# Kernel optimization log

Hardware: AMD Instinct MI355X
Metric: run time of the kernel (lower is better)

Reference implementation:

```python
import jax, jax.numpy as jnp
import numpy as np

EMBED_DIM = 1024
NUM_HEADS = 16
HEAD_DIM = EMBED_DIM // NUM_HEADS


def setup_inputs() -> dict:
    key = jax.random.key(0)
    ks = jax.random.split(key, 9)
    B, T, C = 2, 2048, EMBED_DIM
    s = 1.0 / np.sqrt(C)
    inp = {
        "x": jax.random.normal(ks[0], (B, T, C), dtype=jnp.float32),
        "Wq": jax.random.uniform(ks[1], (C, C), jnp.float32, -s, s),
        "bq": jax.random.uniform(ks[2], (C,), jnp.float32, -s, s),
        "Wk": jax.random.uniform(ks[3], (C, C), jnp.float32, -s, s),
        "bk": jax.random.uniform(ks[4], (C,), jnp.float32, -s, s),
        "Wv": jax.random.uniform(ks[5], (C, C), jnp.float32, -s, s),
        "bv": jax.random.uniform(ks[6], (C,), jnp.float32, -s, s),
        "Wo": jax.random.uniform(ks[7], (C, C), jnp.float32, -s, s),
        "bo": jax.random.uniform(ks[8], (C,), jnp.float32, -s, s),
    }
    return inp


def reference(x, Wq, bq, Wk, bk, Wv, bv, Wo, bo):
    B, T, C = x.shape
    H, D = NUM_HEADS, HEAD_DIM

    def heads(W, b):
        # [B,T,C] -> [B,H,T,D]
        return (x @ W + b).reshape(B, T, H, D).transpose(0, 2, 1, 3)

    q = heads(Wq, bq)
    k = heads(Wk, bk)
    v = heads(Wv, bv)

    scores = jnp.einsum('bhtd,bhsd->bhts', q, k) / np.sqrt(D).astype(np.float32)
    causal = jnp.tril(jnp.ones((T, T), dtype=bool))  # [T,T]
    scores = jnp.where(causal[None, None], scores, -jnp.inf)
    weights = jax.nn.softmax(scores, axis=-1)
    out = jnp.einsum('bhts,bhsd->bhtd', weights, v)  # [B,H,T,D]
    out = out.transpose(0, 2, 1, 3).reshape(B, T, C)
    return out @ Wo + bo
```

## Files before the change

kernel.cpp:

```cpp
#include <hip/hip_runtime.h>
#include <stdint.h>

#define T_LEN 2048
#define C_DIM 1024
#define NHEAD 16
#define HDIM  64
#define MTOT  4096

typedef __bf16 bf16;
typedef __bf16 bf16x4 __attribute__((ext_vector_type(4)));
typedef __bf16 bf16x8 __attribute__((ext_vector_type(8)));
typedef float  f32x4  __attribute__((ext_vector_type(4)));

__device__ __forceinline__ bf16 f2bf(float f) {
    union { float f; unsigned u; } x; x.f = f;
    unsigned r = x.u + 0x7fffu + ((x.u >> 16) & 1u);
    unsigned short h = (unsigned short)(r >> 16);
    return __builtin_bit_cast(bf16, h);
}

__device__ __forceinline__ void g2l16(const void* g, const void* l) {
    __builtin_amdgcn_global_load_lds(
        (const __attribute__((address_space(1))) unsigned int*)(uintptr_t)g,
        (__attribute__((address_space(3))) unsigned int*)(uint32_t)(uintptr_t)l,
        16, 0, 0);
}

__global__ void cast_xw_kernel(const float* __restrict__ x, bf16* __restrict__ xb,
                               const float* __restrict__ W0, const float* __restrict__ W1,
                               const float* __restrict__ W2, const float* __restrict__ W3,
                               bf16* __restrict__ wt) {
    __shared__ float tile[64][68];
    const int tid = threadIdx.x;
    const int bid = blockIdx.x;
    if (bid < 2048) {
        int f = bid * 256 + tid;
        const float4* p = (const float4*)x + (size_t)f * 2;
        float4 a = p[0], b = p[1];
        bf16x8 o;
        o[0] = f2bf(a.x); o[1] = f2bf(a.y); o[2] = f2bf(a.z); o[3] = f2bf(a.w);
        o[4] = f2bf(b.x); o[5] = f2bf(b.y); o[6] = f2bf(b.z); o[7] = f2bf(b.w);
        ((bf16x8*)xb)[f] = o;
        return;
    }
    const int i = bid - 2048;
    const int w = i >> 8;
    const int nt = (i >> 4) & 15;
    const int kt = i & 15;
    const float* W = (w == 0) ? W0 : (w == 1) ? W1 : (w == 2) ? W2 : W3;
    const int kb = kt * 64, nb = nt * 64;
#pragma unroll
    for (int pass = 0; pass < 4; ++pass) {
        int row = pass * 16 + (tid >> 4);
        int col = (tid & 15) * 4;
        float4 v = *(const float4*)(W + (size_t)(kb + row) * 1024 + nb + col);
        *(float4*)(&tile[row][col]) = v;
    }
    __syncthreads();
#pragma unroll
    for (int pass = 0; pass < 2; ++pass) {
        int s = pass * 256 + tid;
        int nn = s >> 3, c = s & 7;
        bf16x8 o;
#pragma unroll
        for (int j = 0; j < 8; ++j) o[j] = f2bf(tile[c * 8 + j][nn]);
        *(bf16x8*)(wt + (size_t)w * 1048576 + (size_t)(nb + nn) * 1024 + kb + c * 8) = o;
    }
}

__global__ void transpose_v_kernel(const bf16* __restrict__ V, bf16* __restrict__ Vtp) {
    __shared__ bf16 tile[128][72];
    const int tid = threadIdx.x;
    const int t0 = blockIdx.x * 128, bh = blockIdx.y;
    const size_t hb = (size_t)bh * 131072;
#pragma unroll
    for (int pass = 0; pass < 4; ++pass) {
        int s = pass * 256 + tid;
        int row = s >> 3, c = s & 7;
        bf16x8 v = *(const bf16x8*)(V + hb + (size_t)(t0 + row) * 64 + c * 8);
        *(bf16x8*)(&tile[row][c * 8]) = v;
    }
    __syncthreads();
#pragma unroll
    for (int pass = 0; pass < 4; ++pass) {
        int s = pass * 256 + tid;
        int d = s >> 4, ch = s & 15;
        bf16x8 o;
#pragma unroll
        for (int j = 0; j < 8; ++j) {
            int orig = 32 * (ch >> 2) + 16 * (j >> 2) + 4 * (ch & 3) + (j & 3);
            o[j] = tile[orig][d];
        }
        *(bf16x8*)(Vtp + hb + (size_t)d * 2048 + t0 + ch * 8) = o;
    }
}

__global__ __launch_bounds__(256, 2)
void gemm_qkv_kernel(const bf16* __restrict__ A, const bf16* __restrict__ Wt,
                     const float* __restrict__ b0, const float* __restrict__ b1,
                     const float* __restrict__ b2, bf16* __restrict__ outQKV) {
    __shared__ char lds[40960];
    bf16* As = (bf16*)lds;
    bf16* Bs = (bf16*)(lds + 16384);

    const int tid = threadIdx.x;
    const int lane = tid & 63, wid = tid >> 6;
    const int r = lane & 15, q4 = lane >> 4;
    const int mbase = blockIdx.y * 128;
    const int nbase = blockIdx.x * 192;
    const int wm = (wid >> 1) * 64;
    const int wn = (wid & 1) * 96;

    f32x4 acc[4][6];
#pragma unroll
    for (int i = 0; i < 4; ++i)
#pragma unroll
        for (int j = 0; j < 6; ++j) acc[i][j] = f32x4{0.f, 0.f, 0.f, 0.f};

    for (int kt = 0; kt < 16; ++kt) {
        int kb = kt * 64;
#pragma unroll
        for (int p = 0; p < 4; ++p) {
            int s = p * 256 + tid;
            int row = s >> 3, blk = s & 7;
            g2l16(A + (size_t)(mbase + row) * 1024 + kb + ((blk ^ (row & 7)) * 8), (char*)As + s * 16);
        }
#pragma unroll
        for (int p = 0; p < 6; ++p) {
            int s = p * 256 + tid;
            int row = s >> 3, blk = s & 7;
            g2l16(Wt + (size_t)(nbase + row) * 1024 + kb + ((blk ^ (row & 7)) * 8), (char*)Bs + s * 16);
        }
        __syncthreads();
#pragma unroll
        for (int ks = 0; ks < 2; ++ks) {
            int blk = ks * 4 + q4;
            bf16x8 a[4], b[6];
#pragma unroll
            for (int i = 0; i < 4; ++i) {
                int rowa = wm + i * 16 + r;
                a[i] = *(const bf16x8*)((const char*)As + rowa * 128 + ((blk ^ (rowa & 7)) * 16));
            }
#pragma unroll
            for (int j = 0; j < 6; ++j) {
                int rowb = wn + j * 16 + r;
                b[j] = *(const bf16x8*)((const char*)Bs + rowb * 128 + ((blk ^ (rowb & 7)) * 16));
            }
#pragma unroll
            for (int i = 0; i < 4; ++i)
#pragma unroll
                for (int j = 0; j < 6; ++j)
                    acc[i][j] = __builtin_amdgcn_mfma_f32_16x16x32_bf16(b[j], a[i], acc[i][j], 0, 0, 0);
        }
        __syncthreads();
    }

    const float QS = 0.18033688011112042f;
#pragma unroll
    for (int i = 0; i < 4; ++i) {
        int m = mbase + wm + i * 16 + r;
        int bi = m >> 11, t = m & 2047;
#pragma unroll
        for (int j = 0; j < 6; ++j) {
            int n0 = nbase + wn + j * 16 + q4 * 4;
            int z = n0 >> 10;
            int nz = n0 & 1023;
            const float* bias = (z == 0) ? b0 : (z == 1) ? b1 : b2;
            float4 bb = *(const float4*)(bias + nz);
            float osc = (z == 0) ? QS : 1.0f;
            bf16x4 w;
            w[0] = f2bf((acc[i][j][0] + bb.x) * osc);
            w[1] = f2bf((acc[i][j][1] + bb.y) * osc);
            w[2] = f2bf((acc[i][j][2] + bb.z) * osc);
            w[3] = f2bf((acc[i][j][3] + bb.w) * osc);
            int h = nz >> 6, d = nz & 63;
            *(bf16x4*)(outQKV + (size_t)z * 4194304 + ((size_t)(bi * 16 + h) * 2048 + t) * 64 + d) = w;
        }
    }
}

__global__ __launch_bounds__(128, 4)
void gemm_o_kernel(const bf16* __restrict__ A, const bf16* __restrict__ Bt,
                   const float* __restrict__ bias, float* __restrict__ out) {
    __shared__ char lds[16384];
    bf16* As = (bf16*)lds;
    bf16* Bs = (bf16*)(lds + 8192);

    const int tid = threadIdx.x;
    const int lane = tid & 63, wid = tid >> 6;
    const int r = lane & 15, q4 = lane >> 4;
    const int nb = blockIdx.x * 64;
    const int mb = blockIdx.y * 64;
    const int wn = wid * 32;

    float4 bvv[2];
#pragma unroll
    for (int j = 0; j < 2; ++j) bvv[j] = *(const float4*)(bias + nb + wn + j * 16 + q4 * 4);

    f32x4 acc[4][2];
#pragma unroll
    for (int i = 0; i < 4; ++i)
#pragma unroll
        for (int j = 0; j < 2; ++j) acc[i][j] = f32x4{0.f, 0.f, 0.f, 0.f};

    for (int kt = 0; kt < 16; ++kt) {
        int kb = kt * 64;
#pragma unroll
        for (int p = 0; p < 4; ++p) {
            int s = p * 128 + tid;
            int row = s >> 3, blk = s & 7;
            g2l16(A + (size_t)(mb + row) * 1024 + kb + ((blk ^ (row & 7)) * 8), (char*)As + s * 16);
        }
#pragma unroll
        for (int p = 0; p < 4; ++p) {
            int s = p * 128 + tid;
            int row = s >> 3, blk = s & 7;
            g2l16(Bt + (size_t)(nb + row) * 1024 + kb + ((blk ^ (row & 7)) * 8), (char*)Bs + s * 16);
        }
        __syncthreads();
#pragma unroll
        for (int ks = 0; ks < 2; ++ks) {
            int blk = ks * 4 + q4;
            bf16x8 a[4], b[2];
#pragma unroll
            for (int i = 0; i < 4; ++i) {
                int rowa = i * 16 + r;
                a[i] = *(const bf16x8*)((const char*)As + rowa * 128 + ((blk ^ (rowa & 7)) * 16));
            }
#pragma unroll
            for (int j = 0; j < 2; ++j) {
                int rowb = wn + j * 16 + r;
                b[j] = *(const bf16x8*)((const char*)Bs + rowb * 128 + ((blk ^ (rowb & 7)) * 16));
            }
#pragma unroll
            for (int i = 0; i < 4; ++i)
#pragma unroll
                for (int j = 0; j < 2; ++j)
                    acc[i][j] = __builtin_amdgcn_mfma_f32_16x16x32_bf16(b[j], a[i], acc[i][j], 0, 0, 0);
        }
        __syncthreads();
    }

#pragma unroll
    for (int i = 0; i < 4; ++i) {
        int m = mb + i * 16 + r;
#pragma unroll
        for (int j = 0; j < 2; ++j) {
            int n0 = nb + wn + j * 16 + q4 * 4;
            float4 w;
            w.x = acc[i][j][0] + bvv[j].x;
            w.y = acc[i][j][1] + bvv[j].y;
            w.z = acc[i][j][2] + bvv[j].z;
            w.w = acc[i][j][3] + bvv[j].w;
            *(float4*)(out + (size_t)m * 1024 + n0) = w;
        }
    }
}

__global__ __launch_bounds__(512, 2)
void attn_kernel(const bf16* __restrict__ Q, const bf16* __restrict__ K,
                 const bf16* __restrict__ Vtp, bf16* __restrict__ Aout) {
    __shared__ char lds[65536];

    const int tid = threadIdx.x, lane = tid & 63, wid = tid >> 6;
    const int r = lane & 15, q4 = lane >> 4;
    const int p = blockIdx.x >> 5;
    const int bh = blockIdx.x & 31;
    const int b = bh >> 4, h = bh & 15;
    const size_t hb = (size_t)bh * 131072;

    const int qi[2] = { p, 15 - p };
    const int ittot = 16 - p;

    bf16x8 qf[2][2];
#pragma unroll
    for (int i = 0; i < 2; ++i)
#pragma unroll
        for (int ks = 0; ks < 2; ++ks) {
            int row = qi[i] * 128 + wid * 16 + r;
            qf[i][ks] = *(const bf16x8*)(Q + hb + (size_t)row * 64 + ks * 32 + q4 * 8);
        }

    bf16x8 ones;
#pragma unroll
    for (int j = 0; j < 8; ++j) ones[j] = (bf16)1.0f;

    f32x4 o[2][4];
    f32x4 osum[2];
#pragma unroll
    for (int i = 0; i < 2; ++i) {
        osum[i] = f32x4{0.f, 0.f, 0.f, 0.f};
#pragma unroll
        for (int jd = 0; jd < 4; ++jd) o[i][jd] = f32x4{0.f, 0.f, 0.f, 0.f};
    }

    auto stage = [&](int buf, int kb) {
        char* Kb = lds + buf * 16384;
        char* Vb = lds + 32768 + buf * 16384;
#pragma unroll
        for (int pp = 0; pp < 2; ++pp) {
            int s = pp * 512 + tid;
            int row = s >> 3, blk = s & 7;
            g2l16(K + hb + (size_t)(kb + row) * 64 + ((blk ^ (row & 7)) * 8), Kb + s * 16);
        }
#pragma unroll
        for (int pp = 0; pp < 2; ++pp) {
            int s = pp * 512 + tid;
            int row = s >> 4, ch = s & 15;
            g2l16(Vtp + hb + (size_t)row * 2048 + kb + ((ch ^ (row & 15)) * 8), Vb + s * 16);
        }
    };

    stage(0, 0);

    for (int it = 0; it < ittot; ++it) {
        __syncthreads();
        const int cb = it & 1;
        if (it + 1 < ittot) stage((it + 1) & 1, (it + 1) * 128);
        const int kb = it * 128;
        const char* Kb = lds + cb * 16384;
        const char* Vb = lds + 32768 + cb * 16384;
        const bool aAct = (it <= qi[0]);

        f32x4 sc[2][8];
#pragma unroll
        for (int st = 0; st < 8; ++st) {
            int rowk = st * 16 + r;
            bf16x8 ak0 = *(const bf16x8*)(Kb + rowk * 128 + ((q4 ^ (rowk & 7)) * 16));
            bf16x8 ak1 = *(const bf16x8*)(Kb + rowk * 128 + (((4 + q4) ^ (rowk & 7)) * 16));
            sc[1][st] = __builtin_amdgcn_mfma_f32_16x16x32_bf16(ak0, qf[1][0], f32x4{0.f, 0.f, 0.f, 0.f}, 0, 0, 0);
            sc[1][st] = __builtin_amdgcn_mfma_f32_16x16x32_bf16(ak1, qf[1][1], sc[1][st], 0, 0, 0);
            if (aAct) {
                sc[0][st] = __builtin_amdgcn_mfma_f32_16x16x32_bf16(ak0, qf[0][0], f32x4{0.f, 0.f, 0.f, 0.f}, 0, 0, 0);
                sc[0][st] = __builtin_amdgcn_mfma_f32_16x16x32_bf16(ak1, qf[0][1], sc[0][st], 0, 0, 0);
            }
        }

#pragma unroll
        for (int i = 0; i < 2; ++i) {
            if (i == 0 && !aAct) continue;
            const bool dia = (it == qi[i]);
            int qrow = qi[i] * 128 + wid * 16 + r;
            bf16x8 pb[4];
#pragma unroll
            for (int c = 0; c < 4; ++c) {
                bf16x8 t;
                if (dia) {
#pragma unroll
                    for (int j = 0; j < 8; ++j) {
                        int st = 2 * c + (j >> 2), reg = j & 3;
                        int key = kb + st * 16 + q4 * 4 + reg;
                        float sv = (key > qrow) ? -1e30f : sc[i][st][reg];
                        t[j] = (bf16)__builtin_amdgcn_exp2f(sv);
                    }
                } else {
#pragma unroll
                    for (int j = 0; j < 8; ++j) {
                        int st = 2 * c + (j >> 2), reg = j & 3;
                        t[j] = (bf16)__builtin_amdgcn_exp2f(sc[i][st][reg]);
                    }
                }
                pb[c] = t;
            }
#pragma unroll
            for (int c = 0; c < 4; ++c) {
                int sidx = c * 4 + q4;
                osum[i] = __builtin_amdgcn_mfma_f32_16x16x32_bf16(ones, pb[c], osum[i], 0, 0, 0);
#pragma unroll
                for (int dsub = 0; dsub < 4; ++dsub) {
                    int rowd = dsub * 16 + r;
                    bf16x8 av = *(const bf16x8*)(Vb + rowd * 256 + ((sidx ^ (rowd & 15)) * 16));
                    o[i][dsub] = __builtin_amdgcn_mfma_f32_16x16x32_bf16(av, pb[c], o[i][dsub], 0, 0, 0);
                }
            }
        }
    }

#pragma unroll
    for (int i = 0; i < 2; ++i) {
        float inv = 1.f / osum[i][0];
        int q = qi[i] * 128 + wid * 16 + r;
#pragma unroll
        for (int dsub = 0; dsub < 4; ++dsub) {
            bf16x4 w;
#pragma unroll
            for (int reg = 0; reg < 4; ++reg) w[reg] = f2bf(o[i][dsub][reg] * inv);
            *(bf16x4*)(Aout + ((size_t)(b * 2048 + q)) * 1024 + h * 64 + dsub * 16 + q4 * 4) = w;
        }
    }
}


extern "C" void kernel_launch(void* const* d_in, const int* in_sizes, int n_in,
                              void* d_out, int out_size, void* d_ws, size_t ws_size,
                              hipStream_t stream) {
    const float* x  = (const float*)d_in[0];
    const float* Wq = (const float*)d_in[1];
    const float* bq = (const float*)d_in[2];
    const float* Wk = (const float*)d_in[3];
    const float* bk = (const float*)d_in[4];
    const float* Wv = (const float*)d_in[5];
    const float* bv = (const float*)d_in[6];
    const float* Wo = (const float*)d_in[7];
    const float* bo = (const float*)d_in[8];
    float* out = (float*)d_out;

    char* ws = (char*)d_ws;
    bf16* xb   = (bf16*)(ws);
    bf16* wt   = (bf16*)(ws + 8388608);
    bf16* qkv  = (bf16*)(ws + 16777216);
    bf16* vtp  = (bf16*)(ws + 41943040);
    bf16* attn = (bf16*)(ws + 50331648);

    hipLaunchKernelGGL(cast_xw_kernel, dim3(3072), dim3(256), 0, stream,
                       x, xb, Wq, Wk, Wv, Wo, wt);
    hipLaunchKernelGGL(gemm_qkv_kernel, dim3(16, 32), dim3(256), 0, stream,
                       xb, wt, bq, bk, bv, qkv);
    hipLaunchKernelGGL(transpose_v_kernel, dim3(16, 32), dim3(256), 0, stream,
                       qkv + (size_t)2 * 4194304, vtp);
    hipLaunchKernelGGL(attn_kernel, dim3(256), dim3(512), 0, stream,
                       qkv, qkv + 4194304, vtp, attn);
    hipLaunchKernelGGL(gemm_o_kernel, dim3(16, 64), dim3(128), 0, stream,
                       attn, wt + (size_t)3 * 1048576, bo, out);
}
```

Measured before the change: 170.7 us.

## Fuse V transpose into QKV GEMM epilogue and shrink attention tiles to 64

The QKV GEMM epilogue now writes V directly in the transposed, permuted layout the attention kernel reads, which removes the separate transpose kernel launch and its round trip through memory. The attention kernel moves from 128-row query/key tiles with 512 threads to 64-row tiles with 256 threads, launching twice as many blocks with half the LDS each. The V epilogue now issues scalar 2-byte strided stores instead of vector stores, and the smaller tiles double the number of loop iterations and barriers.

After: 170.2 us. About the same (-0.3%).

```diff
diff --git a/kernel.cpp b/kernel.cpp
--- a/kernel.cpp
+++ b/kernel.cpp
@@ -68,37 +68,11 @@
     }
 }
 
-__global__ void transpose_v_kernel(const bf16* __restrict__ V, bf16* __restrict__ Vtp) {
-    __shared__ bf16 tile[128][72];
-    const int tid = threadIdx.x;
-    const int t0 = blockIdx.x * 128, bh = blockIdx.y;
-    const size_t hb = (size_t)bh * 131072;
-#pragma unroll
-    for (int pass = 0; pass < 4; ++pass) {
-        int s = pass * 256 + tid;
-        int row = s >> 3, c = s & 7;
-        bf16x8 v = *(const bf16x8*)(V + hb + (size_t)(t0 + row) * 64 + c * 8);
-        *(bf16x8*)(&tile[row][c * 8]) = v;
-    }
-    __syncthreads();
-#pragma unroll
-    for (int pass = 0; pass < 4; ++pass) {
-        int s = pass * 256 + tid;
-        int d = s >> 4, ch = s & 15;
-        bf16x8 o;
-#pragma unroll
-        for (int j = 0; j < 8; ++j) {
-            int orig = 32 * (ch >> 2) + 16 * (j >> 2) + 4 * (ch & 3) + (j & 3);
-            o[j] = tile[orig][d];
-        }
-        *(bf16x8*)(Vtp + hb + (size_t)d * 2048 + t0 + ch * 8) = o;
-    }
-}
-
 __global__ __launch_bounds__(256, 2)
 void gemm_qkv_kernel(const bf16* __restrict__ A, const bf16* __restrict__ Wt,
                      const float* __restrict__ b0, const float* __restrict__ b1,
-                     const float* __restrict__ b2, bf16* __restrict__ outQKV) {
+                     const float* __restrict__ b2, bf16* __restrict__ outQKV,
+                     bf16* __restrict__ Vtp) {
     __shared__ char lds[40960];
     bf16* As = (bf16*)lds;
     bf16* Bs = (bf16*)(lds + 16384);
@@ -167,14 +141,24 @@
             int nz = n0 & 1023;
             const float* bias = (z == 0) ? b0 : (z == 1) ? b1 : b2;
             float4 bb = *(const float4*)(bias + nz);
-            float osc = (z == 0) ? QS : 1.0f;
-            bf16x4 w;
-            w[0] = f2bf((acc[i][j][0] + bb.x) * osc);
-            w[1] = f2bf((acc[i][j][1] + bb.y) * osc);
-            w[2] = f2bf((acc[i][j][2] + bb.z) * osc);
-            w[3] = f2bf((acc[i][j][3] + bb.w) * osc);
             int h = nz >> 6, d = nz & 63;
-            *(bf16x4*)(outQKV + (size_t)z * 4194304 + ((size_t)(bi * 16 + h) * 2048 + t) * 64 + d) = w;
+            if (z == 2) {
+                int tl = t & 127;
+                int tp = (tl & 96) | (((tl >> 2) & 3) << 3) | (((tl >> 4) & 1) << 2) | (tl & 3);
+                size_t base = (size_t)(bi * 16 + h) * 131072 + (size_t)(t & ~127) + tp;
+                Vtp[base + (size_t)(d + 0) * 2048] = f2bf(acc[i][j][0] + bb.x);
+                Vtp[base + (size_t)(d + 1) * 2048] = f2bf(acc[i][j][1] + bb.y);
+                Vtp[base + (size_t)(d + 2) * 2048] = f2bf(acc[i][j][2] + bb.z);
+                Vtp[base + (size_t)(d + 3) * 2048] = f2bf(acc[i][j][3] + bb.w);
+            } else {
+                float osc = (z == 0) ? QS : 1.0f;
+                bf16x4 w;
+                w[0] = f2bf((acc[i][j][0] + bb.x) * osc);
+                w[1] = f2bf((acc[i][j][1] + bb.y) * osc);
+                w[2] = f2bf((acc[i][j][2] + bb.z) * osc);
+                w[3] = f2bf((acc[i][j][3] + bb.w) * osc);
+                *(bf16x4*)(outQKV + (size_t)z * 4194304 + ((size_t)(bi * 16 + h) * 2048 + t) * 64 + d) = w;
+            }
         }
     }
 }
@@ -257,10 +241,10 @@
     }
 }
 
-__global__ __launch_bounds__(512, 2)
+__global__ __launch_bounds__(256, 2)
 void attn_kernel(const bf16* __restrict__ Q, const bf16* __restrict__ K,
                  const bf16* __restrict__ Vtp, bf16* __restrict__ Aout) {
-    __shared__ char lds[65536];
+    __shared__ char lds[32768];
 
     const int tid = threadIdx.x, lane = tid & 63, wid = tid >> 6;
     const int r = lane & 15, q4 = lane >> 4;
@@ -269,15 +253,15 @@
     const int b = bh >> 4, h = bh & 15;
     const size_t hb = (size_t)bh * 131072;
 
-    const int qi[2] = { p, 15 - p };
-    const int ittot = 16 - p;
+    const int qi[2] = { p, 31 - p };
+    const int ittot = 32 - p;
 
     bf16x8 qf[2][2];
 #pragma unroll
     for (int i = 0; i < 2; ++i)
 #pragma unroll
         for (int ks = 0; ks < 2; ++ks) {
-            int row = qi[i] * 128 + wid * 16 + r;
+            int row = qi[i] * 64 + wid * 16 + r;
             qf[i][ks] = *(const bf16x8*)(Q + hb + (size_t)row * 64 + ks * 32 + q4 * 8);
         }
 
@@ -296,18 +280,18 @@
 
     auto stage = [&](int buf, int kb) {
         char* Kb = lds + buf * 16384;
-        char* Vb = lds + 32768 + buf * 16384;
+        char* Vb = Kb + 8192;
 #pragma unroll
         for (int pp = 0; pp < 2; ++pp) {
-            int s = pp * 512 + tid;
+            int s = pp * 256 + tid;
             int row = s >> 3, blk = s & 7;
             g2l16(K + hb + (size_t)(kb + row) * 64 + ((blk ^ (row & 7)) * 8), Kb + s * 16);
         }
 #pragma unroll
         for (int pp = 0; pp < 2; ++pp) {
-            int s = pp * 512 + tid;
-            int row = s >> 4, ch = s & 15;
-            g2l16(Vtp + hb + (size_t)row * 2048 + kb + ((ch ^ (row & 15)) * 8), Vb + s * 16);
+            int s = pp * 256 + tid;
+            int row = s >> 3, ch = s & 7;
+            g2l16(Vtp + hb + (size_t)row * 2048 + kb + ((ch ^ (row & 7)) * 8), Vb + s * 16);
         }
     };
 
@@ -316,15 +300,15 @@
     for (int it = 0; it < ittot; ++it) {
         __syncthreads();
         const int cb = it & 1;
-        if (it + 1 < ittot) stage((it + 1) & 1, (it + 1) * 128);
-        const int kb = it * 128;
+        if (it + 1 < ittot) stage(cb ^ 1, (it + 1) * 64);
+        const int kb = it * 64;
         const char* Kb = lds + cb * 16384;
-        const char* Vb = lds + 32768 + cb * 16384;
+        const char* Vb = Kb + 8192;
         const bool aAct = (it <= qi[0]);
 
-        f32x4 sc[2][8];
-#pragma unroll
-        for (int st = 0; st < 8; ++st) {
+        f32x4 sc[2][4];
+#pragma unroll
+        for (int st = 0; st < 4; ++st) {
             int rowk = st * 16 + r;
             bf16x8 ak0 = *(const bf16x8*)(Kb + rowk * 128 + ((q4 ^ (rowk & 7)) * 16));
             bf16x8 ak1 = *(const bf16x8*)(Kb + rowk * 128 + (((4 + q4) ^ (rowk & 7)) * 16));
@@ -340,10 +324,10 @@
         for (int i = 0; i < 2; ++i) {
             if (i == 0 && !aAct) continue;
             const bool dia = (it == qi[i]);
-            int qrow = qi[i] * 128 + wid * 16 + r;
-            bf16x8 pb[4];
-#pragma unroll
-            for (int c = 0; c < 4; ++c) {
+            int qrow = qi[i] * 64 + wid * 16 + r;
+            bf16x8 pb[2];
+#pragma unroll
+            for (int c = 0; c < 2; ++c) {
                 bf16x8 t;
                 if (dia) {
 #pragma unroll
@@ -363,13 +347,13 @@
                 pb[c] = t;
             }
 #pragma unroll
-            for (int c = 0; c < 4; ++c) {
+            for (int c = 0; c < 2; ++c) {
                 int sidx = c * 4 + q4;
                 osum[i] = __builtin_amdgcn_mfma_f32_16x16x32_bf16(ones, pb[c], osum[i], 0, 0, 0);
 #pragma unroll
                 for (int dsub = 0; dsub < 4; ++dsub) {
                     int rowd = dsub * 16 + r;
-                    bf16x8 av = *(const bf16x8*)(Vb + rowd * 256 + ((sidx ^ (rowd & 15)) * 16));
+                    bf16x8 av = *(const bf16x8*)(Vb + rowd * 128 + ((sidx ^ (rowd & 7)) * 16));
                     o[i][dsub] = __builtin_amdgcn_mfma_f32_16x16x32_bf16(av, pb[c], o[i][dsub], 0, 0, 0);
                 }
             }
@@ -379,7 +363,7 @@
 #pragma unroll
     for (int i = 0; i < 2; ++i) {
         float inv = 1.f / osum[i][0];
-        int q = qi[i] * 128 + wid * 16 + r;
+        int q = qi[i] * 64 + wid * 16 + r;
 #pragma unroll
         for (int dsub = 0; dsub < 4; ++dsub) {
             bf16x4 w;
@@ -415,10 +399,8 @@
     hipLaunchKernelGGL(cast_xw_kernel, dim3(3072), dim3(256), 0, stream,
                        x, xb, Wq, Wk, Wv, Wo, wt);
     hipLaunchKernelGGL(gemm_qkv_kernel, dim3(16, 32), dim3(256), 0, stream,
-                       xb, wt, bq, bk, bv, qkv);
-    hipLaunchKernelGGL(transpose_v_kernel, dim3(16, 32), dim3(256), 0, stream,
-                       qkv + (size_t)2 * 4194304, vtp);
-    hipLaunchKernelGGL(attn_kernel, dim3(256), dim3(512), 0, stream,
+                       xb, wt, bq, bk, bv, qkv, vtp);
+    hipLaunchKernelGGL(attn_kernel, dim3(512), dim3(256), 0, stream,
                        qkv, qkv + 4194304, vtp, attn);
     hipLaunchKernelGGL(gemm_o_kernel, dim3(16, 64), dim3(128), 0, stream,
                        attn, wt + (size_t)3 * 1048576, bo, out);
```
